# Performance work log

Hardware: AMD Instinct MI355X
Metric: run time of the kernel (lower is better)

## Reference

```python
import jax, jax.numpy as jnp
import numpy as np

N = 50000      # nodes
E = 800000     # edges (before self-loops)
F_IN = 512     # input features
H = 8          # heads (layer 1)
C = 32         # hidden per head
CLS = 40       # classes


def setup_inputs() -> dict:
    key = jax.random.key(0)
    ks = jax.random.split(key, 10)
    small = lambda k, shape: jax.random.normal(k, shape, jnp.float32) * 0.05
    return {
        "x": jax.random.normal(ks[0], (N, F_IN), jnp.float32),
        "edge_index": jax.random.randint(ks[1], (2, E), 0, N, jnp.int32),
        # layer 1 params (GATConv: F_IN -> C per head, 8 heads, concat)
        "W1": small(ks[2], (F_IN, H * C)),
        "a_src1": small(ks[3], (H, C)),
        "a_dst1": small(ks[4], (H, C)),
        "b1": jnp.zeros((H * C,), jnp.float32),
        # layer 2 params (GATConv: H*C -> CLS, 1 head)
        "W2": small(ks[5], (H * C, CLS)),
        "a_src2": small(ks[6], (1, CLS)),
        "a_dst2": small(ks[7], (1, CLS)),
        "b2": jnp.zeros((CLS,), jnp.float32),
    }


def gat_conv(x, W, a_src, a_dst, b, src, dst, n):
    """PyG-style GATConv (negative_slope=0.2); self-loops already in src/dst."""
    h_, c_ = a_src.shape
    h = (x @ W).reshape(n, h_, c_)                       # [N, H, C]
    alpha_src = jnp.einsum('nhc,hc->nh', h, a_src)       # [N, H]
    alpha_dst = jnp.einsum('nhc,hc->nh', h, a_dst)       # [N, H]
    e = jax.nn.leaky_relu(alpha_src[src] + alpha_dst[dst], 0.2)  # [E', H]
    # segment softmax over incoming edges of each destination node
    m = jax.lax.stop_gradient(jax.ops.segment_max(e, dst, num_segments=n))
    ex = jnp.exp(e - m[dst])
    den = jax.ops.segment_sum(ex, dst, num_segments=n)
    alpha = ex / (den[dst] + 1e-16)                      # [E', H]
    out = jax.ops.segment_sum(h[src] * alpha[:, :, None], dst, num_segments=n)
    return out.reshape(n, h_ * c_) + b


def reference(x, edge_index, W1, a_src1, a_dst1, b1, W2, a_src2, a_dst2, b2):
    n = x.shape[0]
    loop = jnp.arange(n, dtype=edge_index.dtype)
    src = jnp.concatenate([edge_index[0], loop])  # add self-loops (PyG default)
    dst = jnp.concatenate([edge_index[1], loop])
    # dropout is identity at inference
    h = jax.nn.elu(gat_conv(x, W1, a_src1, a_dst1, b1, src, dst, n))
    out = gat_conv(h, W2, a_src2, a_dst2, b2, src, dst, n)
    return jax.nn.log_softmax(out, axis=1)
```

## Files before the change

kernel.cpp:

```cpp
#include <hip/hip_runtime.h>
#include <hip/hip_bf16.h>
#include <math.h>

constexpr int NN  = 50000;
constexpr int NE  = 800000;
constexpr int EP  = NE + NN;
constexpr int FIN = 512;
constexpr int NH  = 8;
constexpr int NC  = 32;
constexpr int HC  = NH * NC;
constexpr int CLS = 40;
constexpr int CLSP = 48;
constexpr int NGB  = (NN + 63) / 64;
constexpr int NSCB = (EP + 255) / 256;
constexpr int DEGB = (NN + 255) / 256;
constexpr int CVTW_ITEMS = HC * (FIN / 8) + CLSP * HC;
constexpr int CVTW_B = (CVTW_ITEMS + 255) / 256;

typedef __attribute__((ext_vector_type(8))) __bf16 bf16x8;
typedef __attribute__((ext_vector_type(4))) __bf16 bf16x4;
typedef __attribute__((ext_vector_type(4))) float f32x4;
typedef __attribute__((ext_vector_type(2))) float f32x2;

__device__ inline bf16x8 cvt8v(const f32x4 a, const f32x4 b) {
  bf16x8 o;
  o[0] = (__bf16)a.x; o[1] = (__bf16)a.y; o[2] = (__bf16)a.z; o[3] = (__bf16)a.w;
  o[4] = (__bf16)b.x; o[5] = (__bf16)b.y; o[6] = (__bf16)b.z; o[7] = (__bf16)b.w;
  return o;
}

__device__ inline unsigned char to_fp8(float f) {
  int pk = __builtin_amdgcn_cvt_pk_fp8_f32(f, f, 0, false);
  return (unsigned char)(pk & 0xff);
}

__device__ inline float from_fp8(unsigned char b) {
  f32x2 v = __builtin_amdgcn_cvt_pk_f32_fp8((unsigned)b, false);
  return v.x;
}

__global__ void k_pre0(int* __restrict__ deg,
                       const float* __restrict__ W1, const float* __restrict__ W2,
                       __bf16* __restrict__ Wt, __bf16* __restrict__ W2t) {
  if (blockIdx.x < DEGB) {
    int i = blockIdx.x * 256 + threadIdx.x;
    if (i < NN) deg[i] = 0;
    return;
  }
  int t = (blockIdx.x - DEGB) * 256 + threadIdx.x;
  if (t < HC * (FIN / 8)) {
    int c = t >> 6, kq = (t & 63) * 8;
    bf16x8 o;
#pragma unroll
    for (int j = 0; j < 8; ++j) o[j] = (__bf16)W1[(size_t)(kq + j) * HC + c];
    *(bf16x8*)&Wt[(size_t)c * FIN + kq] = o;
  } else if (t < CVTW_ITEMS) {
    int u = t - HC * (FIN / 8);
    int c = u >> 8, k = u & 255;
    W2t[u] = (c < CLS) ? (__bf16)W2[(size_t)k * CLS + c] : (__bf16)0.f;
  }
}

__global__ __launch_bounds__(256) void k_gemm1_hist(
    const float* __restrict__ X, const __bf16* __restrict__ Wt,
    const float* __restrict__ a_s1, const float* __restrict__ a_d1,
    unsigned char* __restrict__ Hout, float* __restrict__ asrc1,
    float* __restrict__ adst1,
    const int* __restrict__ ei, int* __restrict__ deg,
    int* __restrict__ rank) {
  __shared__ __align__(16) float Xp[2][4096];
  const int tid = threadIdx.x;

  if (blockIdx.x >= NGB) {
    int e = (blockIdx.x - NGB) * 256 + tid;
    if (e < EP) {
      int d = (e < NE) ? ei[NE + e] : (e - NE);
      rank[e] = atomicAdd(&deg[d], 1);
    }
    return;
  }

  const int lane = tid & 63;
  const int w    = tid >> 6;
  const int wn   = w * 64;
  const int bm   = blockIdx.x * 64;
  const int l15  = lane & 15, lg = lane >> 4;

  const int srow_l  = (lane >> 4);
  const int sslot   = (l15 >> 1);
  const int shalf   = (lane & 1);

  f32x4 acc[4][4] = {};

  auto issue = [&](int c, int buf) {
#pragma unroll
    for (int jj = 0; jj < 4; ++jj) {
      const int j = w * 4 + jj;
      const int row_l = 4 * j + srow_l;
      const int rowG = min(bm + row_l, NN - 1);
      const int g = sslot ^ (row_l & 7);
      const float* src = X + (size_t)rowG * FIN + c * 64 + g * 8 + shalf * 4;
      __builtin_amdgcn_global_load_lds(
          (const __attribute__((address_space(1))) void*)src,
          (__attribute__((address_space(3))) void*)(&Xp[buf][j * 256]), 16, 0, 0);
    }
  };

  issue(0, 0);
  for (int c = 0; c < 8; ++c) {
    const int cur = c & 1;
    __syncthreads();
    if (c < 7) issue(c + 1, cur ^ 1);

#pragma unroll
    for (int kh = 0; kh < 2; ++kh) {
      const int kb = lg + 4 * kh;
      bf16x8 bv[4];
#pragma unroll
      for (int ni = 0; ni < 4; ++ni)
        bv[ni] = *(const bf16x8*)(Wt + (size_t)(wn + ni * 16 + l15) * FIN
                                     + c * 64 + kb * 8);
#pragma unroll
      for (int mi = 0; mi < 4; ++mi) {
        int r = mi * 16 + l15;
        int fo = r * 64 + ((kb ^ (r & 7)) << 3);
        f32x4 alo = *(const f32x4*)&Xp[cur][fo];
        f32x4 ahi = *(const f32x4*)&Xp[cur][fo + 4];
        bf16x8 av = cvt8v(alo, ahi);
#pragma unroll
        for (int ni = 0; ni < 4; ++ni)
          acc[mi][ni] = __builtin_amdgcn_mfma_f32_16x16x32_bf16(
              av, bv[ni], acc[mi][ni], 0, 0, 0);
      }
    }
  }

  const int hbase = 2 * w;
#pragma unroll
  for (int hh = 0; hh < 2; ++hh) {
    float asA = a_s1[(hbase + hh) * NC + l15];
    float asB = a_s1[(hbase + hh) * NC + 16 + l15];
    float adA = a_d1[(hbase + hh) * NC + l15];
    float adB = a_d1[(hbase + hh) * NC + 16 + l15];
    float vs = 0.f, vd = 0.f;
#pragma unroll
    for (int mi = 0; mi < 4; ++mi) {
#pragma unroll
      for (int r = 0; r < 4; ++r) {
        float ps = acc[mi][2 * hh][r] * asA + acc[mi][2 * hh + 1][r] * asB;
        float pd = acc[mi][2 * hh][r] * adA + acc[mi][2 * hh + 1][r] * adB;
#pragma unroll
        for (int off = 1; off < 16; off <<= 1) {
          ps += __shfl_xor(ps, off, 64);
          pd += __shfl_xor(pd, off, 64);
        }
        if (l15 == mi * 4 + r) { vs = ps; vd = pd; }
      }
    }
    int rw = bm + (l15 >> 2) * 16 + lg * 4 + (l15 & 3);
    if (rw < NN) {
      asrc1[(size_t)rw * NH + hbase + hh] = vs;
      adst1[(size_t)rw * NH + hbase + hh] = vd;
    }
  }

#pragma unroll
  for (int mi = 0; mi < 4; ++mi) {
#pragma unroll
    for (int ni = 0; ni < 4; ++ni) {
      int col = wn + ni * 16 + l15;
#pragma unroll
      for (int r = 0; r < 4; ++r) {
        int row = bm + mi * 16 + lg * 4 + r;
        if (row < NN) Hout[(size_t)row * HC + col] = to_fp8(acc[mi][ni][r]);
      }
    }
  }
}

__global__ __launch_bounds__(1024) void k_scan1(const int* __restrict__ deg,
                                                int* __restrict__ rowptr1,
                                                int* __restrict__ bsum, int n) {
  __shared__ int sm[1024];
  int i = blockIdx.x * 1024 + threadIdx.x;
  int v = (i < n) ? deg[i] : 0;
  sm[threadIdx.x] = v;
  __syncthreads();
  for (int off = 1; off < 1024; off <<= 1) {
    int t = (threadIdx.x >= off) ? sm[threadIdx.x - off] : 0;
    __syncthreads();
    sm[threadIdx.x] += t;
    __syncthreads();
  }
  if (i < n) rowptr1[i] = sm[threadIdx.x];
  if (threadIdx.x == 1023) bsum[blockIdx.x] = sm[1023];
}

__global__ void k_scan23(int* __restrict__ rowptr, const int* __restrict__ bsum,
                         int nb, int n) {
  __shared__ int off[64];
  if (threadIdx.x < 64) {
    int lane = threadIdx.x;
    int v = (lane < nb) ? bsum[lane] : 0;
#pragma unroll
    for (int o = 1; o < 64; o <<= 1) {
      int t = __shfl_up(v, o);
      if (lane >= o) v += t;
    }
    int ex = __shfl_up(v, 1);
    if (lane == 0) ex = 0;
    off[lane] = ex;
  }
  __syncthreads();
  int i = blockIdx.x * 256 + threadIdx.x;
  if (i == 0) rowptr[0] = 0;
  if (i < n) rowptr[i + 1] += off[i >> 10];
}

__global__ void k_pass2(const int* __restrict__ ei, const int* __restrict__ rank,
                        const int* __restrict__ rowptr,
                        unsigned short* __restrict__ srcS) {
  int e = blockIdx.x * 256 + threadIdx.x;
  if (e >= EP) return;
  int s, d;
  if (e < NE) { s = ei[e]; d = ei[NE + e]; } else { s = d = e - NE; }
  srcS[rowptr[d] + rank[e]] = (unsigned short)s;
}

__global__ __launch_bounds__(256) void k_agg1(const unsigned char* __restrict__ h1f8,
                                              const float* __restrict__ asrc,
                                              const float* __restrict__ adst,
                                              const unsigned short* __restrict__ srcS,
                                              const int* __restrict__ rowptr,
                                              const float* __restrict__ b1,
                                              __bf16* __restrict__ helu) {
  int wave = (blockIdx.x * 256 + threadIdx.x) >> 6;
  int lane = threadIdx.x & 63;
  if (wave >= NN) return;
  int lo = rowptr[wave], hi = rowptr[wave + 1];
  int head = lane >> 3;
  int hw   = lane & 7;
  float adstv = adst[wave * NH + head];
  float ad2   = adst[wave * NH + hw];
  float4 acc = {0.f, 0.f, 0.f, 0.f};
  float den = 0.f;

  for (int base = lo; base < hi; base += 64) {
    int cnt = hi - base; if (cnt > 64) cnt = 64;
    int sv = (lane < cnt) ? (int)srcS[base + lane] : 0;
    int j = 0;
    for (; j + 8 <= cnt; j += 8) {
      int se = __shfl(sv, j + head);
      float v = asrc[se * NH + hw] + ad2;
      v = v > 0.f ? v : 0.2f * v;
      float wv = __expf(v);
      int s[8]; unsigned int hv[8];
#pragma unroll
      for (int u = 0; u < 8; ++u) s[u] = __shfl(sv, j + u);
#pragma unroll
      for (int u = 0; u < 8; ++u)
        hv[u] = *(const unsigned int*)&h1f8[(size_t)s[u] * HC + lane * 4];
#pragma unroll
      for (int u = 0; u < 8; ++u) {
        float wu = __shfl(wv, u * 8 + head);
        f32x2 lo2 = __builtin_amdgcn_cvt_pk_f32_fp8(hv[u], false);
        f32x2 hi2 = __builtin_amdgcn_cvt_pk_f32_fp8(hv[u], true);
        acc.x += wu * lo2.x;
        acc.y += wu * lo2.y;
        acc.z += wu * hi2.x;
        acc.w += wu * hi2.y;
        den += wu;
      }
    }
    for (; j < cnt; ++j) {
      int s = __shfl(sv, j);
      float v = asrc[s * NH + head] + adstv;
      v = v > 0.f ? v : 0.2f * v;
      float w = __expf(v);
      unsigned int hv = *(const unsigned int*)&h1f8[(size_t)s * HC + lane * 4];
      f32x2 lo2 = __builtin_amdgcn_cvt_pk_f32_fp8(hv, false);
      f32x2 hi2 = __builtin_amdgcn_cvt_pk_f32_fp8(hv, true);
      acc.x += w * lo2.x;
      acc.y += w * lo2.y;
      acc.z += w * hi2.x;
      acc.w += w * hi2.y;
      den += w;
    }
  }

  float inv = 1.f / (den + 1e-16f);
  float4 bb = *(const float4*)&b1[lane * 4];
  float o[4] = {acc.x * inv + bb.x, acc.y * inv + bb.y,
                acc.z * inv + bb.z, acc.w * inv + bb.w};
  bf16x4 ov;
#pragma unroll
  for (int j2 = 0; j2 < 4; ++j2) {
    float e = o[j2] > 0.f ? o[j2] : expm1f(o[j2]);
    ov[j2] = (__bf16)e;
  }
  *(bf16x4*)&helu[(size_t)wave * HC + lane * 4] = ov;
}

__global__ __launch_bounds__(256) void k_gemm2m(const __bf16* __restrict__ A,
                                                const __bf16* __restrict__ W2t,
                                                const float* __restrict__ a_s2,
                                                const float* __restrict__ a_d2,
                                                unsigned char* __restrict__ h2p,
                                                float* __restrict__ asrc2,
                                                float* __restrict__ adst2) {
  __shared__ __align__(16) __bf16 As[128 * 8 * 8];
  __shared__ __align__(16) __bf16 Bsh[CLSP * 33 * 8];
  const int tid  = threadIdx.x;
  const int lane = tid & 63;
  const int w    = tid >> 6;
  const int wm   = w * 32;
  const int bm   = blockIdx.x * 128;

  const int l3 = lane >> 3;
  const int l7 = lane & 7;
  const int kb_src = l7 ^ l3;

  for (int s = tid; s < CLSP * 32; s += 256) {
    int c = s >> 5, kb = s & 31;
    *(bf16x8*)(Bsh + (size_t)(c * 33 + kb) * 8) =
        *(const bf16x8*)(W2t + (size_t)c * HC + kb * 8);
  }

  f32x4 acc[2][3] = {};

  for (int step = 0; step < 4; ++step) {
    const int k0 = step * 64;
#pragma unroll
    for (int q = 0; q < 4; ++q) {
      const int inst = w * 4 + q;
      const int r = inst * 8 + l3;
      const int arow = min(bm + r, NN - 1);
      const __bf16* ga = A + (size_t)arow * HC + k0 + kb_src * 8;
      __builtin_amdgcn_global_load_lds(
          (const __attribute__((address_space(1))) void*)ga,
          (__attribute__((address_space(3))) void*)(As + inst * 512), 16, 0, 0);
    }
    __syncthreads();

    const int l15 = lane & 15, lg = lane >> 4;
#pragma unroll
    for (int kh = 0; kh < 2; ++kh) {
      const int kbl = lg + 4 * kh;
      const int kbg = step * 8 + kbl;
      bf16x8 av[2], bv[3];
#pragma unroll
      for (int mi = 0; mi < 2; ++mi) {
        int r = wm + mi * 16 + l15;
        av[mi] = *(const bf16x8*)(As + (size_t)(r * 8 + (kbl ^ (r & 7))) * 8);
      }
#pragma unroll
      for (int ni = 0; ni < 3; ++ni) {
        int c = ni * 16 + l15;
        bv[ni] = *(const bf16x8*)(Bsh + (size_t)(c * 33 + kbg) * 8);
      }
#pragma unroll
      for (int mi = 0; mi < 2; ++mi)
#pragma unroll
        for (int ni = 0; ni < 3; ++ni)
          acc[mi][ni] = __builtin_amdgcn_mfma_f32_16x16x32_bf16(
              av[mi], bv[ni], acc[mi][ni], 0, 0, 0);
    }
    __syncthreads();
  }

  const int l15 = lane & 15, lg = lane >> 4;

  {
    int c0 = l15, c1 = 16 + l15, c2 = 32 + l15;
    float as0 = a_s2[c0], as1 = a_s2[c1], as2v = (c2 < CLS) ? a_s2[c2] : 0.f;
    float ad0 = a_d2[c0], ad1 = a_d2[c1], ad2v = (c2 < CLS) ? a_d2[c2] : 0.f;
    float vs = 0.f, vd = 0.f;
#pragma unroll
    for (int mi = 0; mi < 2; ++mi) {
#pragma unroll
      for (int r = 0; r < 4; ++r) {
        float ps = acc[mi][0][r] * as0 + acc[mi][1][r] * as1 + acc[mi][2][r] * as2v;
        float pd = acc[mi][0][r] * ad0 + acc[mi][1][r] * ad1 + acc[mi][2][r] * ad2v;
#pragma unroll
        for (int off = 1; off < 16; off <<= 1) {
          ps += __shfl_xor(ps, off, 64);
          pd += __shfl_xor(pd, off, 64);
        }
        if (l15 == mi * 4 + r) { vs = ps; vd = pd; }
      }
    }
    int rw = bm + wm + (l15 >> 2) * 16 + lg * 4 + (l15 & 3);
    if (l15 < 8 && rw < NN) {
      asrc2[rw] = vs;
      adst2[rw] = vd;
    }
  }

#pragma unroll
  for (int mi = 0; mi < 2; ++mi) {
#pragma unroll
    for (int ni = 0; ni < 3; ++ni) {
      int col = ni * 16 + l15;
      if (col >= CLS) continue;
#pragma unroll
      for (int r = 0; r < 4; ++r) {
        int row = bm + wm + mi * 16 + lg * 4 + r;
        if (row < NN) h2p[(size_t)row * 64 + col] = to_fp8(acc[mi][ni][r]);
      }
    }
  }
}

__global__ __launch_bounds__(256) void k_agg2(const unsigned char* __restrict__ h2p,
                                              const float* __restrict__ asrc,
                                              const float* __restrict__ adst,
                                              const unsigned short* __restrict__ srcS,
                                              const int* __restrict__ rowptr,
                                              const float* __restrict__ b2,
                                              float* __restrict__ out) {
  int wave = (blockIdx.x * 256 + threadIdx.x) >> 6;
  int lane = threadIdx.x & 63;
  if (wave >= NN) return;
  int lo = rowptr[wave], hi = rowptr[wave + 1];
  bool act = lane < CLS;
  float adstv = adst[wave];
  float acc = 0.f, den = 0.f;

  for (int base = lo; base < hi; base += 64) {
    int cnt = hi - base; if (cnt > 64) cnt = 64;
    int sv = (lane < cnt) ? (int)srcS[base + lane] : 0;
    float v = asrc[sv] + adstv;
    v = v > 0.f ? v : 0.2f * v;
    float wv = __expf(v);
    int j = 0;
    for (; j + 8 <= cnt; j += 8) {
      int s[8]; float hval[8];
#pragma unroll
      for (int u = 0; u < 8; ++u) s[u] = __shfl(sv, j + u);
#pragma unroll
      for (int u = 0; u < 8; ++u)
        hval[u] = act ? from_fp8(h2p[(size_t)s[u] * 64 + lane]) : 0.f;
#pragma unroll
      for (int u = 0; u < 8; ++u) {
        float wu = __shfl(wv, j + u);
        acc += wu * hval[u];
        den += wu;
      }
    }
    for (; j < cnt; ++j) {
      int s = __shfl(sv, j);
      float wu = __shfl(wv, j);
      if (act) acc += wu * from_fp8(h2p[(size_t)s * 64 + lane]);
      den += wu;
    }
  }

  float o = act ? (acc / (den + 1e-16f) + b2[lane]) : -INFINITY;
  float m = o;
#pragma unroll
  for (int off = 32; off; off >>= 1) m = fmaxf(m, __shfl_xor(m, off, 64));
  float ex = act ? __expf(o - m) : 0.f;
  float ssum = ex;
#pragma unroll
  for (int off = 32; off; off >>= 1) ssum += __shfl_xor(ssum, off, 64);
  if (act) out[(size_t)wave * CLS + lane] = o - m - logf(ssum);
}

extern "C" void kernel_launch(void* const* d_in, const int* in_sizes, int n_in,
                              void* d_out, int out_size, void* d_ws, size_t ws_size,
                              hipStream_t stream) {
  const float* x      = (const float*)d_in[0];
  const int*   ei     = (const int*)d_in[1];
  const float* W1     = (const float*)d_in[2];
  const float* a_src1 = (const float*)d_in[3];
  const float* a_dst1 = (const float*)d_in[4];
  const float* b1     = (const float*)d_in[5];
  const float* W2     = (const float*)d_in[6];
  const float* a_src2 = (const float*)d_in[7];
  const float* a_dst2 = (const float*)d_in[8];
  const float* b2     = (const float*)d_in[9];
  float* out = (float*)d_out;

  char* p = (char*)d_ws;
  auto alloc = [&](size_t bytes) {
    char* r = p;
    p += (bytes + 255) & ~size_t(255);
    return r;
  };
  unsigned char* h1f8 = (unsigned char*)alloc((size_t)NN * HC);
  __bf16* helu  = (__bf16*)alloc((size_t)NN * HC * 2);
  __bf16* Wt    = (__bf16*)alloc((size_t)HC * FIN * 2);
  __bf16* W2t   = (__bf16*)alloc((size_t)CLSP * HC * 2);
  unsigned char* h2p = (unsigned char*)alloc((size_t)NN * 64);
  float*  asrc1 = (float*)alloc((size_t)NN * NH * 4);
  float*  adst1 = (float*)alloc((size_t)NN * NH * 4);
  float*  asrc2 = (float*)alloc((size_t)NN * 4);
  float*  adst2 = (float*)alloc((size_t)NN * 4);
  unsigned short* srcS = (unsigned short*)alloc((size_t)EP * 2);
  int*    rank  = (int*)alloc((size_t)EP * 4);
  int*    deg   = (int*)alloc((size_t)NN * 4);
  int*    rowptr= (int*)alloc((size_t)(NN + 1) * 4);
  int*    bsum  = (int*)alloc(256 * 4);

  const int nbScan = (NN + 1023) / 1024;

  k_pre0<<<DEGB + CVTW_B, 256, 0, stream>>>(deg, W1, W2, Wt, W2t);

  k_gemm1_hist<<<NGB + NSCB, 256, 0, stream>>>(x, Wt, a_src1, a_dst1,
                                               h1f8, asrc1, adst1,
                                               ei, deg, rank);

  k_scan1<<<nbScan, 1024, 0, stream>>>(deg, rowptr + 1, bsum, NN);
  k_scan23<<<(NN + 255) / 256, 256, 0, stream>>>(rowptr, bsum, nbScan, NN);

  k_pass2<<<NSCB, 256, 0, stream>>>(ei, rank, rowptr, srcS);

  k_agg1<<<(NN + 3) / 4, 256, 0, stream>>>(h1f8, asrc1, adst1, srcS, rowptr, b1, helu);

  k_gemm2m<<<(NN + 127) / 128, 256, 0, stream>>>(helu, W2t, a_src2, a_dst2,
                                                 h2p, asrc2, adst2);

  k_agg2<<<(NN + 3) / 4, 256, 0, stream>>>(h2p, asrc2, adst2, srcS, rowptr, b2, out);
}
```

Before: 192.0 us.

## Interleave GEMM and histogram blocks, halve GEMM K-chunk, drop self-loop atomics

The fused GEMM1/degree-histogram kernel now interleaves one GEMM block with every four histogram blocks in the grid, so the atomic histogram work runs alongside the GEMM instead of trailing it. The GEMM K-chunk is halved from 64 to 32, using 16 pipeline stages with half the LDS per block to allow higher occupancy. Self-loop edges are no longer counted with atomics: the scan adds one to each degree, and pass2 places the self-loop in the last slot of each row. This shrinks the rank buffer and the atomic traffic, at the cost of more loop iterations and barriers in the GEMM.

```diff
diff --git a/kernel.cpp b/kernel.cpp
--- a/kernel.cpp
+++ b/kernel.cpp
@@ -12,7 +12,9 @@
 constexpr int CLS = 40;
 constexpr int CLSP = 48;
 constexpr int NGB  = (NN + 63) / 64;
-constexpr int NSCB = (EP + 255) / 256;
+constexpr int NHB  = (NE + 255) / 256;
+constexpr int NFB  = NGB + NHB;
+constexpr int NP2B = (EP + 255) / 256;
 constexpr int DEGB = (NN + 255) / 256;
 constexpr int CVTW_ITEMS = HC * (FIN / 8) + CLSP * HC;
 constexpr int CVTW_B = (CVTW_ITEMS + 255) / 256;
@@ -68,38 +70,40 @@
     float* __restrict__ adst1,
     const int* __restrict__ ei, int* __restrict__ deg,
     int* __restrict__ rank) {
-  __shared__ __align__(16) float Xp[2][4096];
+  __shared__ __align__(16) float Xp[2][2048];
   const int tid = threadIdx.x;
-
-  if (blockIdx.x >= NGB) {
-    int e = (blockIdx.x - NGB) * 256 + tid;
-    if (e < EP) {
-      int d = (e < NE) ? ei[NE + e] : (e - NE);
+  const int bid = blockIdx.x;
+  const bool isGemm = (bid % 5 == 0) && (bid < 5 * NGB);
+
+  if (!isGemm) {
+    int hb = (bid < 5 * NGB) ? (bid - bid / 5 - 1) : (bid - NGB);
+    int e = hb * 256 + tid;
+    if (e < NE) {
+      int d = ei[NE + e];
       rank[e] = atomicAdd(&deg[d], 1);
     }
     return;
   }
 
+  const int gb   = bid / 5;
   const int lane = tid & 63;
   const int w    = tid >> 6;
   const int wn   = w * 64;
-  const int bm   = blockIdx.x * 64;
+  const int bm   = gb * 64;
   const int l15  = lane & 15, lg = lane >> 4;
 
-  const int srow_l  = (lane >> 4);
-  const int sslot   = (l15 >> 1);
-  const int shalf   = (lane & 1);
+  const int srow_l = (lane >> 3);
+  const int sslot  = (lane & 7) ^ (lane >> 3);
 
   f32x4 acc[4][4] = {};
 
   auto issue = [&](int c, int buf) {
 #pragma unroll
-    for (int jj = 0; jj < 4; ++jj) {
-      const int j = w * 4 + jj;
-      const int row_l = 4 * j + srow_l;
+    for (int jj = 0; jj < 2; ++jj) {
+      const int j = w * 2 + jj;
+      const int row_l = 8 * j + srow_l;
       const int rowG = min(bm + row_l, NN - 1);
-      const int g = sslot ^ (row_l & 7);
-      const float* src = X + (size_t)rowG * FIN + c * 64 + g * 8 + shalf * 4;
+      const float* src = X + (size_t)rowG * FIN + c * 32 + sslot * 4;
       __builtin_amdgcn_global_load_lds(
           (const __attribute__((address_space(1))) void*)src,
           (__attribute__((address_space(3))) void*)(&Xp[buf][j * 256]), 16, 0, 0);
@@ -107,31 +111,29 @@
   };
 
   issue(0, 0);
-  for (int c = 0; c < 8; ++c) {
+  for (int c = 0; c < 16; ++c) {
     const int cur = c & 1;
     __syncthreads();
-    if (c < 7) issue(c + 1, cur ^ 1);
-
-#pragma unroll
-    for (int kh = 0; kh < 2; ++kh) {
-      const int kb = lg + 4 * kh;
-      bf16x8 bv[4];
+    if (c < 15) issue(c + 1, cur ^ 1);
+
+    const int kb = lg;
+    bf16x8 bv[4];
+#pragma unroll
+    for (int ni = 0; ni < 4; ++ni)
+      bv[ni] = *(const bf16x8*)(Wt + (size_t)(wn + ni * 16 + l15) * FIN
+                                   + c * 32 + kb * 8);
+#pragma unroll
+    for (int mi = 0; mi < 4; ++mi) {
+      int r = mi * 16 + l15;
+      int p0 = (2 * kb) ^ (r & 7);
+      int p1 = (2 * kb + 1) ^ (r & 7);
+      f32x4 alo = *(const f32x4*)&Xp[cur][r * 32 + p0 * 4];
+      f32x4 ahi = *(const f32x4*)&Xp[cur][r * 32 + p1 * 4];
+      bf16x8 av = cvt8v(alo, ahi);
 #pragma unroll
       for (int ni = 0; ni < 4; ++ni)
-        bv[ni] = *(const bf16x8*)(Wt + (size_t)(wn + ni * 16 + l15) * FIN
-                                     + c * 64 + kb * 8);
-#pragma unroll
-      for (int mi = 0; mi < 4; ++mi) {
-        int r = mi * 16 + l15;
-        int fo = r * 64 + ((kb ^ (r & 7)) << 3);
-        f32x4 alo = *(const f32x4*)&Xp[cur][fo];
-        f32x4 ahi = *(const f32x4*)&Xp[cur][fo + 4];
-        bf16x8 av = cvt8v(alo, ahi);
-#pragma unroll
-        for (int ni = 0; ni < 4; ++ni)
-          acc[mi][ni] = __builtin_amdgcn_mfma_f32_16x16x32_bf16(
-              av, bv[ni], acc[mi][ni], 0, 0, 0);
-      }
+        acc[mi][ni] = __builtin_amdgcn_mfma_f32_16x16x32_bf16(
+            av, bv[ni], acc[mi][ni], 0, 0, 0);
     }
   }
 
@@ -183,7 +185,7 @@
                                                 int* __restrict__ bsum, int n) {
   __shared__ int sm[1024];
   int i = blockIdx.x * 1024 + threadIdx.x;
-  int v = (i < n) ? deg[i] : 0;
+  int v = (i < n) ? deg[i] + 1 : 0;
   sm[threadIdx.x] = v;
   __syncthreads();
   for (int off = 1; off < 1024; off <<= 1) {
@@ -222,9 +224,13 @@
                         unsigned short* __restrict__ srcS) {
   int e = blockIdx.x * 256 + threadIdx.x;
   if (e >= EP) return;
-  int s, d;
-  if (e < NE) { s = ei[e]; d = ei[NE + e]; } else { s = d = e - NE; }
-  srcS[rowptr[d] + rank[e]] = (unsigned short)s;
+  if (e < NE) {
+    int s = ei[e], d = ei[NE + e];
+    srcS[rowptr[d] + rank[e]] = (unsigned short)s;
+  } else {
+    int d = e - NE;
+    srcS[rowptr[d + 1] - 1] = (unsigned short)d;
+  }
 }
 
 __global__ __launch_bounds__(256) void k_agg1(const unsigned char* __restrict__ h1f8,
@@ -497,7 +503,7 @@
   float*  asrc2 = (float*)alloc((size_t)NN * 4);
   float*  adst2 = (float*)alloc((size_t)NN * 4);
   unsigned short* srcS = (unsigned short*)alloc((size_t)EP * 2);
-  int*    rank  = (int*)alloc((size_t)EP * 4);
+  int*    rank  = (int*)alloc((size_t)NE * 4);
   int*    deg   = (int*)alloc((size_t)NN * 4);
   int*    rowptr= (int*)alloc((size_t)(NN + 1) * 4);
   int*    bsum  = (int*)alloc(256 * 4);
@@ -506,14 +512,14 @@
 
   k_pre0<<<DEGB + CVTW_B, 256, 0, stream>>>(deg, W1, W2, Wt, W2t);
 
-  k_gemm1_hist<<<NGB + NSCB, 256, 0, stream>>>(x, Wt, a_src1, a_dst1,
-                                               h1f8, asrc1, adst1,
-                                               ei, deg, rank);
+  k_gemm1_hist<<<NFB, 256, 0, stream>>>(x, Wt, a_src1, a_dst1,
+                                        h1f8, asrc1, adst1,
+                                        ei, deg, rank);
 
   k_scan1<<<nbScan, 1024, 0, stream>>>(deg, rowptr + 1, bsum, NN);
   k_scan23<<<(NN + 255) / 256, 256, 0, stream>>>(rowptr, bsum, nbScan, NN);
 
-  k_pass2<<<NSCB, 256, 0, stream>>>(ei, rank, rowptr, srcS);
+  k_pass2<<<NP2B, 256, 0, stream>>>(ei, rank, rowptr, srcS);
 
   k_agg1<<<(NN + 3) / 4, 256, 0, stream>>>(h1f8, asrc1, adst1, srcS, rowptr, b1, helu);
 
```

Measured after the change: 195.2 us. Within noise of the previous version (+1.7%).
